# Kernel tuning notes

Hardware: AMD Instinct MI355X
Metric: run time of the kernel (lower is better)

## Reference

```python
import jax, jax.numpy as jnp
import numpy as np

B, T, D, S, EXP = 4, 2048, 1024, 16, 2
E = D * EXP  # expanded channels = 2048


def setup_inputs() -> dict:
    key = jax.random.key(0)
    ks = jax.random.split(key, 8)
    s = 0.02
    f = jnp.float32
    return {
        "x": jax.random.normal(ks[0], (B, T, D), f),
        "in_w": jax.random.normal(ks[1], (2 * E, D), f) * s,
        "in_b": jnp.zeros((2 * E,), f),
        "conv_w": jax.random.normal(ks[2], (E, 1, 3), f) * s,  # depthwise conv, groups=E
        "conv_b": jnp.zeros((E,), f),
        "dt_w": jax.random.normal(ks[3], (E, E), f) * s,
        "dt_b": jnp.zeros((E,), f),
        "B_w": jax.random.normal(ks[4], (S, E), f) * s,
        "B_b": jnp.zeros((S,), f),
        "C_w": jax.random.normal(ks[5], (S, E), f) * s,
        "C_b": jnp.zeros((S,), f),
        "D_w": jax.random.normal(ks[6], (S, E), f) * s,
        "D_b": jnp.zeros((S,), f),
        "out_w": jax.random.normal(ks[7], (D, E), f) * s,
        "out_b": jnp.zeros((D,), f),
    }


def reference(x, in_w, in_b, conv_w, conv_b, dt_w, dt_b, B_w, B_b, C_w, C_b, D_w, D_b, out_w, out_b):
    silu = jax.nn.silu
    # in_proj -> split into main / gate, each [B,T,E]
    xp = x @ in_w.T + in_b
    x_main, x_gate = xp[..., :E], xp[..., E:]
    # depthwise temporal conv (kernel 3, pad 1, groups=E), then SiLU
    xc = jax.lax.conv_general_dilated(
        x_main.transpose(0, 2, 1), conv_w, (1,), [(1, 1)],
        dimension_numbers=("NCH", "OIH", "NCH"), feature_group_count=E)
    xc = silu((xc + conv_b[None, :, None]).transpose(0, 2, 1))  # [B,T,E]
    dt = jax.nn.softplus(xc @ dt_w.T + dt_b)                     # [B,T,E]
    Bt = xc @ B_w.T + B_b                                        # [B,T,S]
    Ct = xc @ C_w.T + C_b
    Dt = xc @ D_w.T + D_b
    decay = jnp.exp(jnp.clip(-dt.mean(-1), -10.0, 10.0))         # [B,T] scalar decay per step
    u = Bt * Dt                                                  # [B,T,S] state input

    def step(state, inp):  # state [B,S]
        d, u_t, c_t = inp
        state = state * d[:, None] + u_t
        return state, (c_t * state).sum(-1)  # y_t [B]

    _, ys = jax.lax.scan(step, jnp.zeros((x.shape[0], S), x.dtype),
                         (decay.T, u.transpose(1, 0, 2), Ct.transpose(1, 0, 2)))
    y = ys.T[..., None] * silu(x_gate)  # broadcast [B,T,1] -> [B,T,E] (matches .expand)
    return x + (y @ out_w.T + out_b)    # dropout in eval mode = identity
```

## Files before the change

### kernel.cpp

```cpp
#include <hip/hip_runtime.h>
#include <hip/hip_bf16.h>

#define Bsz 4
#define Tsz 2048
#define Dsz 1024
#define Ssz 16
#define Esz 2048
#define Mrows (Bsz*Tsz)

typedef __attribute__((ext_vector_type(8))) short short8;
typedef __attribute__((ext_vector_type(4))) float floatx4;
typedef __attribute__((ext_vector_type(8))) int int8v;
typedef __attribute__((ext_vector_type(4))) int int4v;

__device__ __forceinline__ void async_ld16(const void* g, void* l) {
    __builtin_amdgcn_global_load_lds(
        (const __attribute__((address_space(1))) void*)g,
        (__attribute__((address_space(3))) void*)l,
        16, 0, 0);
}

__device__ __forceinline__ float sigmoidf_(float v) { return 1.f / (1.f + expf(-v)); }
__device__ __forceinline__ float bf2f(unsigned short u) {
    union { unsigned u32; float f; } c; c.u32 = (unsigned)u << 16; return c.f;
}
__device__ __forceinline__ int pk_fp8x4(float a, float b, float c, float d) {
    int lo = __builtin_amdgcn_cvt_pk_fp8_f32(a, b, 0, 0);
    int hi = __builtin_amdgcn_cvt_pk_fp8_f32(c, d, 0, 0);
    return (lo & 0xFFFF) | (hi << 16);
}

#define WAIT_VM(N)   (0xF70 | (N))
#define WAIT_LGKM(N) (0xC07F | ((N) << 8))

#define CV_S0 2097152
#define CV_S1 3145728
#define CV_S2 4194304
#define CV_S3 4718592
__global__ void cvt_all(const float4* __restrict__ x,  const float4* __restrict__ iw,
                        const float4* __restrict__ dw, const float4* __restrict__ ow,
                        int* __restrict__ x8, int* __restrict__ iw8,
                        int* __restrict__ dw8, int* __restrict__ ow8) {
    int i = blockIdx.x * blockDim.x + threadIdx.x;
    const int stride = gridDim.x * blockDim.x;
    for (; i < CV_S3; i += stride) {
        if (i < CV_S0) {
            float4 v = x[i];
            x8[i] = pk_fp8x4(v.x, v.y, v.z, v.w);
        } else if (i < CV_S1) {
            const int j = i - CV_S0;
            float4 v = iw[j];
            iw8[j] = pk_fp8x4(v.x * 64.f, v.y * 64.f, v.z * 64.f, v.w * 64.f);
        } else if (i < CV_S2) {
            const int j = i - CV_S1;
            float4 v = dw[j];
            dw8[j] = pk_fp8x4(v.x * 64.f, v.y * 64.f, v.z * 64.f, v.w * 64.f);
        } else {
            const int j = i - CV_S2;
            float4 v = ow[j];
            ow8[j] = pk_fp8x4(v.x * 64.f, v.y * 64.f, v.z * 64.f, v.w * 64.f);
        }
    }
}

template<int MODE, int SA, int SB>
__launch_bounds__(256, 2)
__global__ void gemm_f8(const unsigned char* __restrict__ A,
                        const unsigned char* __restrict__ Bw,
                        const float* __restrict__ bias,
                        int M, int N, int K,
                        __hip_bfloat16* __restrict__ outb,
                        float* __restrict__ rowsum,
                        const float* __restrict__ resid,
                        const float* __restrict__ ysv,
                        float* __restrict__ outf) {
    __shared__ __align__(16) unsigned char sA[2 * 16384];
    __shared__ __align__(16) unsigned char sB[2 * 16384];

    const int tid  = threadIdx.x;
    const int wave = tid >> 6, lane = tid & 63;
    const int wm = wave >> 1, wn = wave & 1;
    const int q = lane >> 4, lr = lane & 15;

    const int gx = gridDim.x, gy = gridDim.y;
    const int flat = blockIdx.y * gx + blockIdx.x;
    const int stripe = gy >> 3;
    const int xcd = flat & 7, local = flat >> 3;
    const int mt = xcd * stripe + (local % stripe);
    const int nt = local / stripe;
    const int m0 = mt * 128, n0 = nt * 128;

    floatx4 acc[4][4];
#pragma unroll
    for (int i = 0; i < 4; ++i)
#pragma unroll
        for (int j = 0; j < 4; ++j) acc[i][j] = (floatx4){0.f, 0.f, 0.f, 0.f};

    const unsigned char* pa[4];
    const unsigned char* pb[4];
#pragma unroll
    for (int i = 0; i < 4; ++i) {
        const int idx = i * 256 + tid, row = idx >> 3, s = idx & 7;
        pa[i] = A + (size_t)(m0 + row) * K + ((s ^ (row & 7)) * 16);
        pb[i] = Bw + (size_t)(n0 + row) * K + ((s ^ (row & 7)) * 16);
    }

    const int rA = wm * 64 + lr, rB = wn * 64 + lr;
    const int oA0 = rA * 128 + (((2 * q)     ^ (rA & 7)) * 16);
    const int oA1 = rA * 128 + (((2 * q + 1) ^ (rA & 7)) * 16);
    const int oB0 = rB * 128 + (((2 * q)     ^ (rB & 7)) * 16);
    const int oB1 = rB * 128 + (((2 * q + 1) ^ (rB & 7)) * 16);

#define F8_ISSUE(ST) do {                                                      \
        _Pragma("unroll")                                                      \
        for (int i = 0; i < 4; ++i) {                                          \
            async_ld16(pa[i], &sA[(ST) * 16384 + (i * 256 + wave * 64) * 16]); \
            pa[i] += 128;                                                      \
        }                                                                      \
        _Pragma("unroll")                                                      \
        for (int i = 0; i < 4; ++i) {                                          \
            async_ld16(pb[i], &sB[(ST) * 16384 + (i * 256 + wave * 64) * 16]); \
            pb[i] += 128;                                                      \
        }                                                                      \
    } while (0)

#define F8_STEP(ST) do {                                                       \
        asm volatile("" ::: "memory");                                         \
        __builtin_amdgcn_s_waitcnt(WAIT_VM(8));          \
        __builtin_amdgcn_s_barrier();                                          \
        asm volatile("" ::: "memory");                                         \
        int8v a8[4], b8[4];                                                    \
        _Pragma("unroll")                                                      \
        for (int i = 0; i < 4; ++i) {                                          \
            int4v lo = *(const int4v*)&sA[(ST) * 16384 + oA0 + i * 2048];      \
            int4v hi = *(const int4v*)&sA[(ST) * 16384 + oA1 + i * 2048];      \
            a8[i] = __builtin_shufflevector(lo, hi, 0, 1, 2, 3, 4, 5, 6, 7);   \
        }                                                                      \
        _Pragma("unroll")                                                      \
        for (int j = 0; j < 4; ++j) {                                          \
            int4v lo = *(const int4v*)&sB[(ST) * 16384 + oB0 + j * 2048];      \
            int4v hi = *(const int4v*)&sB[(ST) * 16384 + oB1 + j * 2048];      \
            b8[j] = __builtin_shufflevector(lo, hi, 0, 1, 2, 3, 4, 5, 6, 7);   \
        }                                                                      \
        asm volatile("" ::: "memory");                                         \
        __builtin_amdgcn_s_waitcnt(WAIT_LGKM(0));            \
        __builtin_amdgcn_s_barrier();                      \
        asm volatile("" ::: "memory");                                         \
        F8_ISSUE(ST);                               \
        _Pragma("unroll")                                                      \
        for (int i = 0; i < 4; ++i)                                            \
            _Pragma("unroll")                                                  \
            for (int j = 0; j < 4; ++j)                                        \
                acc[i][j] = __builtin_amdgcn_mfma_scale_f32_16x16x128_f8f6f4(  \
                    a8[i], b8[j], acc[i][j], 0, 0, 0, SA, 0, SB);              \
    } while (0)

    const int nit = K >> 8;
    F8_ISSUE(0);
    F8_ISSUE(1);
    for (int it = 0; it < nit; ++it) {
        F8_STEP(0);
        F8_STEP(1);
    }
#undef F8_STEP
#undef F8_ISSUE
    asm volatile("" ::: "memory");
    __builtin_amdgcn_s_waitcnt(WAIT_VM(0));

    if (MODE == 0) {
#pragma unroll
        for (int i = 0; i < 4; ++i) {
            const int row = m0 + wm * 64 + i * 16 + q * 4;
#pragma unroll
            for (int j = 0; j < 4; ++j) {
                const int col = n0 + wn * 64 + j * 16 + lr;
                const float bc = bias[col];
#pragma unroll
                for (int r = 0; r < 4; ++r)
                    outb[(size_t)(row + r) * N + col] = __float2bfloat16(acc[i][j][r] + bc);
            }
        }
    } else if (MODE == 1) {
#pragma unroll
        for (int i = 0; i < 4; ++i) {
            float rs[4] = {0.f, 0.f, 0.f, 0.f};
#pragma unroll
            for (int j = 0; j < 4; ++j) {
                const int col = n0 + wn * 64 + j * 16 + lr;
                const float bc = bias[col];
#pragma unroll
                for (int r = 0; r < 4; ++r) {
                    float v = acc[i][j][r] + bc;
                    float sp = (v > 20.f) ? v : log1pf(expf(v));
                    rs[r] += sp;
                }
            }
#pragma unroll
            for (int r = 0; r < 4; ++r) {
                float v = rs[r];
                v += __shfl_xor(v, 1); v += __shfl_xor(v, 2);
                v += __shfl_xor(v, 4); v += __shfl_xor(v, 8);
                if (lr == 0)
                    atomicAdd(&rowsum[m0 + wm * 64 + i * 16 + q * 4 + r], v);
            }
        }
    } else {
#pragma unroll
        for (int i = 0; i < 4; ++i) {
            const int row = m0 + wm * 64 + i * 16 + q * 4;
#pragma unroll
            for (int j = 0; j < 4; ++j) {
                const int col = n0 + wn * 64 + j * 16 + lr;
                const float bc = bias[col];
#pragma unroll
                for (int r = 0; r < 4; ++r) {
                    const size_t idx = (size_t)(row + r) * N + col;
                    outf[idx] = resid[idx] + ysv[row + r] * acc[i][j][r] + bc;
                }
            }
        }
    }
}

__global__ void conv_gate_k(const __hip_bfloat16* __restrict__ xp,
                            const float* __restrict__ cw,
                            const float* __restrict__ cb,
                            __hip_bfloat16* __restrict__ xc,
                            int2* __restrict__ xc8,
                            int2* __restrict__ s8) {
    const int idx8 = blockIdx.x * blockDim.x + threadIdx.x;
    const int e = (idx8 & (Esz / 8 - 1)) * 8;
    const int r = idx8 >> 8;
    const int t = r & (Tsz - 1);
    const unsigned short* row0 = (const unsigned short*)(xp + (size_t)r * (2 * Esz) + e);
    short8 vm1 = (t > 0)       ? *(const short8*)(row0 - 2 * Esz) : (short8){0,0,0,0,0,0,0,0};
    short8 v00 = *(const short8*)row0;
    short8 vp1 = (t < Tsz - 1) ? *(const short8*)(row0 + 2 * Esz) : (short8){0,0,0,0,0,0,0,0};
    short8 o;
    float sil[8];
#pragma unroll
    for (int k = 0; k < 8; ++k) {
        const int ek = e + k;
        float v = bf2f((unsigned short)vm1[k]) * cw[ek * 3 + 0]
                + bf2f((unsigned short)v00[k]) * cw[ek * 3 + 1]
                + bf2f((unsigned short)vp1[k]) * cw[ek * 3 + 2] + cb[ek];
        sil[k] = v * sigmoidf_(v);
        __hip_bfloat16 h = __float2bfloat16(sil[k]);
        o[k] = *(short*)&h;
    }
    *(short8*)(xc + (size_t)idx8 * 8) = o;
    int2 p;
    p.x = pk_fp8x4(sil[0] * 16.f, sil[1] * 16.f, sil[2] * 16.f, sil[3] * 16.f);
    p.y = pk_fp8x4(sil[4] * 16.f, sil[5] * 16.f, sil[6] * 16.f, sil[7] * 16.f);
    xc8[idx8] = p;

    short8 g = *(const short8*)(row0 + Esz);
    float sg[8];
#pragma unroll
    for (int k = 0; k < 8; ++k) {
        const float gv = bf2f((unsigned short)g[k]);
        sg[k] = gv * sigmoidf_(gv);
    }
    int2 ps;
    ps.x = pk_fp8x4(sg[0] * 16.f, sg[1] * 16.f, sg[2] * 16.f, sg[3] * 16.f);
    ps.y = pk_fp8x4(sg[4] * 16.f, sg[5] * 16.f, sg[6] * 16.f, sg[7] * 16.f);
    s8[idx8] = ps;
}

__global__ void pack_bcd(const float* __restrict__ Bw, const float* __restrict__ Cw,
                         const float* __restrict__ Dw, __hip_bfloat16* __restrict__ Wb) {
    const int idx = blockIdx.x * blockDim.x + threadIdx.x;
    if (idx >= 48 * Esz) return;
    const int row = idx >> 11, col = idx & (Esz - 1);
    float v;
    if (row < 16)      v = Bw[row * Esz + col];
    else if (row < 32) v = Cw[(row - 16) * Esz + col];
    else               v = Dw[(row - 32) * Esz + col];
    Wb[idx] = __float2bfloat16(v);
}

__launch_bounds__(128)
__global__ void bcd_mfma2(const __hip_bfloat16* __restrict__ xc,
                          const __hip_bfloat16* __restrict__ Wb,
                          const float* __restrict__ Bb, const float* __restrict__ Cb,
                          const float* __restrict__ Db,
                          float* __restrict__ u, float* __restrict__ Ct) {
    __shared__ __align__(16) __hip_bfloat16 sW[48 * 256];
    const int tid = threadIdx.x;
    const int wave = tid >> 6, lane = tid & 63;
    const int q = lane >> 4, lr = lane & 15;
    const int m0 = blockIdx.x * 32;

    floatx4 acc[3];
#pragma unroll
    for (int j = 0; j < 3; ++j) acc[j] = (floatx4){0.f, 0.f, 0.f, 0.f};

    const __hip_bfloat16* arow = xc + (size_t)(m0 + wave * 16 + lr) * Esz;

    for (int kt = 0; kt < 8; ++kt) {
        const int k0 = kt << 8;
        __syncthreads();
#pragma unroll
        for (int j = 0; j < 12; ++j) {
            const int idx = j * 128 + tid;
            const int row = idx >> 5, ch = idx & 31;
            async_ld16(&Wb[(size_t)row * Esz + k0 + ch * 8],
                       (__hip_bfloat16*)sW + idx * 8);
        }
        __builtin_amdgcn_s_waitcnt(WAIT_VM(0));
        __syncthreads();

        short8 af[8];
#pragma unroll
        for (int ks = 0; ks < 8; ++ks)
            af[ks] = *(const short8*)&arow[k0 + ks * 32 + q * 8];
#pragma unroll
        for (int ks = 0; ks < 8; ++ks) {
#pragma unroll
            for (int j = 0; j < 3; ++j) {
                short8 wf = *(const short8*)&sW[(j * 16 + lr) * 256 + ks * 32 + q * 8];
                acc[j] = __builtin_amdgcn_mfma_f32_16x16x32_bf16(af[ks], wf, acc[j], 0, 0, 0);
            }
        }
    }

    const int row = m0 + wave * 16 + q * 4;
    const float bb = Bb[lr], cbv = Cb[lr], db = Db[lr];
#pragma unroll
    for (int r = 0; r < 4; ++r) {
        const float bt = acc[0][r] + bb;
        const float ct = acc[1][r] + cbv;
        const float dt = acc[2][r] + db;
        u [(size_t)(row + r) * Ssz + lr] = bt * dt;
        Ct[(size_t)(row + r) * Ssz + lr] = ct;
    }
}

__global__ void scanA(const float* __restrict__ rowsum, const float* __restrict__ u,
                      const float* __restrict__ Ct,
                      float* __restrict__ ysl, float* __restrict__ pt,
                      float* __restrict__ send) {
    const int cid = blockIdx.x;
    const int b = cid >> 3, c = cid & 7;
    const int t0 = c * 256;
    const int tid = threadIdx.x;
    const int lane = tid & 63, wave = tid >> 6;
    __shared__ __align__(16) float su[256 * Ssz];
    __shared__ __align__(16) float sc[256 * Ssz];
    __shared__ float sp[256 * 17];
    __shared__ float sd[256];

    const float4* ub = (const float4*)(u  + ((size_t)b * Tsz + t0) * Ssz);
    const float4* cb = (const float4*)(Ct + ((size_t)b * Tsz + t0) * Ssz);
#pragma unroll
    for (int i = 0; i < 4; ++i) {
        ((float4*)su)[tid + i * 256] = ub[tid + i * 256];
        ((float4*)sc)[tid + i * 256] = cb[tid + i * 256];
    }
    {
        const float m = rowsum[b * Tsz + t0 + tid] * (1.f / (float)Esz);
        sd[tid] = expf(fminf(fmaxf(-m, -10.f), 10.f));
    }
    __syncthreads();
    if (wave == 0 && lane < 16) {
        float st = 0.f, P = 1.f;
#pragma unroll 8
        for (int i = 0; i < 256; ++i) {
            const float d = sd[i];
            st = st * d + su[i * Ssz + lane];
            sp[i * 17 + lane] = sc[i * Ssz + lane] * st;
            if (lane == 0) { P *= d; sp[i * 17 + 16] = P; }
        }
        send[cid * Ssz + lane] = st;
    }
    __syncthreads();
    float s = 0.f;
#pragma unroll
    for (int j = 0; j < 16; ++j) s += sp[tid * 17 + j];
    ysl[b * Tsz + t0 + tid] = s;
    pt [b * Tsz + t0 + tid] = sp[tid * 17 + 16];
}

__global__ void scanB(const float* __restrict__ send, const float* __restrict__ pt,
                      float* __restrict__ sstart) {
    const int tid = threadIdx.x;
    if (tid >= 64) return;
    const int b = tid >> 4, j = tid & 15;
    float s = 0.f;
    for (int c = 0; c < 8; ++c) {
        const int cid = b * 8 + c;
        sstart[cid * Ssz + j] = s;
        const float Pc = pt[b * Tsz + c * 256 + 255];
        s = send[cid * Ssz + j] + Pc * s;
    }
}

__global__ void scanC(const float* __restrict__ ysl, const float* __restrict__ pt,
                      const float* __restrict__ sstart, const float* __restrict__ Ct,
                      float* __restrict__ ys) {
    const int cid = blockIdx.x;
    const int b = cid >> 3, c = cid & 7;
    const int t0 = c * 256;
    const int tid = threadIdx.x;
    __shared__ float s0[Ssz];
    if (tid < 16) s0[tid] = sstart[cid * Ssz + tid];
    __syncthreads();
    const int g = b * Tsz + t0 + tid;
    const float4* cr = (const float4*)(Ct + (size_t)g * Ssz);
    float dot = 0.f;
#pragma unroll
    for (int i = 0; i < 4; ++i) {
        float4 v = cr[i];
        dot += v.x * s0[i * 4 + 0] + v.y * s0[i * 4 + 1]
             + v.z * s0[i * 4 + 2] + v.w * s0[i * 4 + 3];
    }
    ys[g] = ysl[g] + pt[g] * dot;
}

extern "C" void kernel_launch(void* const* d_in, const int* in_sizes, int n_in,
                              void* d_out, int out_size, void* d_ws, size_t ws_size,
                              hipStream_t stream) {
    const float* x      = (const float*)d_in[0];
    const float* in_w   = (const float*)d_in[1];
    const float* in_b   = (const float*)d_in[2];
    const float* conv_w = (const float*)d_in[3];
    const float* conv_b = (const float*)d_in[4];
    const float* dt_w   = (const float*)d_in[5];
    const float* dt_b   = (const float*)d_in[6];
    const float* B_w    = (const float*)d_in[7];
    const float* B_b    = (const float*)d_in[8];
    const float* C_w    = (const float*)d_in[9];
    const float* C_b    = (const float*)d_in[10];
    const float* D_w    = (const float*)d_in[11];
    const float* D_b    = (const float*)d_in[12];
    const float* out_w  = (const float*)d_in[13];
    const float* out_b  = (const float*)d_in[14];
    float* out = (float*)d_out;

    char* ws = (char*)d_ws;
    auto alloc = [&](size_t bytes) {
        char* p = ws;
        ws += (bytes + 255) & ~(size_t)255;
        return p;
    };
    unsigned char* x_f8    = (unsigned char*)alloc((size_t)Mrows * Dsz);
    unsigned char* inw_f8  = (unsigned char*)alloc((size_t)2 * Esz * Dsz);
    unsigned char* dtw_f8  = (unsigned char*)alloc((size_t)Esz * Esz);
    unsigned char* outw_f8 = (unsigned char*)alloc((size_t)Dsz * Esz);
    __hip_bfloat16* xp_bf  = (__hip_bfloat16*)alloc((size_t)Mrows * 2 * Esz * 2);
    __hip_bfloat16* xc_bf  = (__hip_bfloat16*)alloc((size_t)Mrows * Esz * 2);
    unsigned char* xc_f8   = (unsigned char*)alloc((size_t)Mrows * Esz);
    unsigned char* s_f8    = (unsigned char*)alloc((size_t)Mrows * Esz);
    __hip_bfloat16* wb_bf  = (__hip_bfloat16*)alloc((size_t)48 * Esz * 2);
    float* rowsum = (float*)alloc(Mrows * 4);
    float* u_buf  = (float*)alloc((size_t)Mrows * Ssz * 4);
    float* ct_buf = (float*)alloc((size_t)Mrows * Ssz * 4);
    float* ys_buf = (float*)alloc(Mrows * 4);
    float* ysl_buf = (float*)alloc(Mrows * 4);
    float* pt_buf  = (float*)alloc(Mrows * 4);
    float* send_buf = (float*)alloc(32 * Ssz * 4);
    float* sstart_buf = (float*)alloc(32 * Ssz * 4);
    (void)alloc(65536);

    hipMemsetAsync(rowsum, 0, Mrows * 4, stream);

    cvt_all<<<4608, 256, 0, stream>>>((const float4*)x, (const float4*)in_w,
                                      (const float4*)dt_w, (const float4*)out_w,
                                      (int*)x_f8, (int*)inw_f8, (int*)dtw_f8,
                                      (int*)outw_f8);
    pack_bcd<<<48 * Esz / 256, 256, 0, stream>>>(B_w, C_w, D_w, wb_bf);

    gemm_f8<0, 127, 121><<<dim3(4096 / 128, Mrows / 128), 256, 0, stream>>>(
        x_f8, inw_f8, in_b, Mrows, 4096, 1024, xp_bf, nullptr, nullptr, nullptr, nullptr);

    conv_gate_k<<<(Mrows * Esz / 8) / 256, 256, 0, stream>>>(
        xp_bf, conv_w, conv_b, xc_bf, (int2*)xc_f8, (int2*)s_f8);

    gemm_f8<1, 123, 121><<<dim3(Esz / 128, Mrows / 128), 256, 0, stream>>>(
        xc_f8, dtw_f8, dt_b, Mrows, Esz, Esz, nullptr, rowsum, nullptr, nullptr, nullptr);

    bcd_mfma2<<<Mrows / 32, 128, 0, stream>>>(xc_bf, wb_bf, B_b, C_b, D_b, u_buf, ct_buf);

    scanA<<<32, 256, 0, stream>>>(rowsum, u_buf, ct_buf, ysl_buf, pt_buf, send_buf);
    scanB<<<1, 64, 0, stream>>>(send_buf, pt_buf, sstart_buf);
    scanC<<<32, 256, 0, stream>>>(ysl_buf, pt_buf, sstart_buf, ct_buf, ys_buf);

    gemm_f8<2, 123, 121><<<dim3(Dsz / 128, Mrows / 128), 256, 0, stream>>>(
        s_f8, outw_f8, out_b, Mrows, Dsz, Esz, nullptr, nullptr, x, ys_buf, out);
}
```

Before: 385.7 us.

## Fuse gate SiLU into in_proj epilogue, merge weight packing and scan passes

The in_proj GEMM now writes only the main half as bf16 and applies SiLU plus fp8 quantisation to the gate half directly in its epilogue. This removes the bf16 round trip of the gate columns and the gate work in the conv kernel. The B/C/D weight packing is folded into the conversion kernel, and the single-block scanB is removed by having each scanC block recompute its chunk start state serially. The changes cut kernel launches and intermediate memory traffic. The cost is byte-wide scattered fp8 stores in the GEMM epilogue.

New measurement: 380.6 us. Within noise of the previous version (-1.3%).

```diff
diff --git a/kernel.cpp b/kernel.cpp
--- a/kernel.cpp
+++ b/kernel.cpp
@@ -12,6 +12,7 @@
 typedef __attribute__((ext_vector_type(4))) float floatx4;
 typedef __attribute__((ext_vector_type(8))) int int8v;
 typedef __attribute__((ext_vector_type(4))) int int4v;
+typedef __attribute__((ext_vector_type(4))) unsigned short ushort4v;
 
 __device__ __forceinline__ void async_ld16(const void* g, void* l) {
     __builtin_amdgcn_global_load_lds(
@@ -24,6 +25,10 @@
 __device__ __forceinline__ float bf2f(unsigned short u) {
     union { unsigned u32; float f; } c; c.u32 = (unsigned)u << 16; return c.f;
 }
+__device__ __forceinline__ unsigned short f2bf(float f) {
+    __hip_bfloat16 h = __float2bfloat16(f);
+    return *(unsigned short*)&h;
+}
 __device__ __forceinline__ int pk_fp8x4(float a, float b, float c, float d) {
     int lo = __builtin_amdgcn_cvt_pk_fp8_f32(a, b, 0, 0);
     int hi = __builtin_amdgcn_cvt_pk_fp8_f32(c, d, 0, 0);
@@ -37,13 +42,17 @@
 #define CV_S1 3145728
 #define CV_S2 4194304
 #define CV_S3 4718592
+#define CV_S4 4743168
 __global__ void cvt_all(const float4* __restrict__ x,  const float4* __restrict__ iw,
                         const float4* __restrict__ dw, const float4* __restrict__ ow,
+                        const float4* __restrict__ Bw, const float4* __restrict__ Cw,
+                        const float4* __restrict__ Dw,
                         int* __restrict__ x8, int* __restrict__ iw8,
-                        int* __restrict__ dw8, int* __restrict__ ow8) {
+                        int* __restrict__ dw8, int* __restrict__ ow8,
+                        ushort4v* __restrict__ wb) {
     int i = blockIdx.x * blockDim.x + threadIdx.x;
     const int stride = gridDim.x * blockDim.x;
-    for (; i < CV_S3; i += stride) {
+    for (; i < CV_S4; i += stride) {
         if (i < CV_S0) {
             float4 v = x[i];
             x8[i] = pk_fp8x4(v.x, v.y, v.z, v.w);
@@ -55,10 +64,19 @@
             const int j = i - CV_S1;
             float4 v = dw[j];
             dw8[j] = pk_fp8x4(v.x * 64.f, v.y * 64.f, v.z * 64.f, v.w * 64.f);
-        } else {
+        } else if (i < CV_S3) {
             const int j = i - CV_S2;
             float4 v = ow[j];
             ow8[j] = pk_fp8x4(v.x * 64.f, v.y * 64.f, v.z * 64.f, v.w * 64.f);
+        } else {
+            const int j = i - CV_S3;
+            float4 v;
+            if (j < 8192)       v = Bw[j];
+            else if (j < 16384) v = Cw[j - 8192];
+            else                v = Dw[j - 16384];
+            ushort4v o;
+            o[0] = f2bf(v.x); o[1] = f2bf(v.y); o[2] = f2bf(v.z); o[3] = f2bf(v.w);
+            wb[j] = o;
         }
     }
 }
@@ -73,7 +91,8 @@
                         float* __restrict__ rowsum,
                         const float* __restrict__ resid,
                         const float* __restrict__ ysv,
-                        float* __restrict__ outf) {
+                        float* __restrict__ outf,
+                        unsigned char* __restrict__ gate8) {
     __shared__ __align__(16) unsigned char sA[2 * 16384];
     __shared__ __align__(16) unsigned char sB[2 * 16384];
 
@@ -204,7 +223,7 @@
                     atomicAdd(&rowsum[m0 + wm * 64 + i * 16 + q * 4 + r], v);
             }
         }
-    } else {
+    } else if (MODE == 2) {
 #pragma unroll
         for (int i = 0; i < 4; ++i) {
             const int row = m0 + wm * 64 + i * 16 + q * 4;
@@ -219,23 +238,56 @@
                 }
             }
         }
-    }
-}
-
-__global__ void conv_gate_k(const __hip_bfloat16* __restrict__ xp,
+    } else {
+        if (nt < 16) {
+#pragma unroll
+            for (int i = 0; i < 4; ++i) {
+                const int row = m0 + wm * 64 + i * 16 + q * 4;
+#pragma unroll
+                for (int j = 0; j < 4; ++j) {
+                    const int col = n0 + wn * 64 + j * 16 + lr;
+                    const float bc = bias[col];
+#pragma unroll
+                    for (int r = 0; r < 4; ++r)
+                        outb[(size_t)(row + r) * Esz + col] =
+                            __float2bfloat16(acc[i][j][r] + bc);
+                }
+            }
+        } else {
+#pragma unroll
+            for (int i = 0; i < 4; ++i) {
+                const int row = m0 + wm * 64 + i * 16 + q * 4;
+#pragma unroll
+                for (int j = 0; j < 4; ++j) {
+                    const int col = n0 + wn * 64 + j * 16 + lr;
+                    const float bc = bias[col];
+                    const int colg = col - Esz;
+#pragma unroll
+                    for (int r = 0; r < 4; ++r) {
+                        const float v = acc[i][j][r] + bc;
+                        const float sil = v * sigmoidf_(v) * 16.f;
+                        const int pk = __builtin_amdgcn_cvt_pk_fp8_f32(sil, sil, 0, 0);
+                        gate8[(size_t)(row + r) * Esz + colg] = (unsigned char)(pk & 0xFF);
+                    }
+                }
+            }
+        }
+    }
+}
+
+__global__ void conv_gate_k(const __hip_bfloat16* __restrict__ xpm,
                             const float* __restrict__ cw,
                             const float* __restrict__ cb,
                             __hip_bfloat16* __restrict__ xc,
-                            int2* __restrict__ xc8,
-                            int2* __restrict__ s8) {
+                            int2* __restrict__ xc8) {
     const int idx8 = blockIdx.x * blockDim.x + threadIdx.x;
     const int e = (idx8 & (Esz / 8 - 1)) * 8;
     const int r = idx8 >> 8;
     const int t = r & (Tsz - 1);
-    const unsigned short* row0 = (const unsigned short*)(xp + (size_t)r * (2 * Esz) + e);
-    short8 vm1 = (t > 0)       ? *(const short8*)(row0 - 2 * Esz) : (short8){0,0,0,0,0,0,0,0};
+    const unsigned short* row0 = (const unsigned short*)(xpm + (size_t)r * Esz + e);
+    short8 vm1 = (t > 0)       ? *(const short8*)(row0 - Esz) : (short8){0,0,0,0,0,0,0,0};
     short8 v00 = *(const short8*)row0;
-    short8 vp1 = (t < Tsz - 1) ? *(const short8*)(row0 + 2 * Esz) : (short8){0,0,0,0,0,0,0,0};
+    short8 vp1 = (t < Tsz - 1) ? *(const short8*)(row0 + Esz) : (short8){0,0,0,0,0,0,0,0};
     short8 o;
     float sil[8];
 #pragma unroll
@@ -245,38 +297,13 @@
                 + bf2f((unsigned short)v00[k]) * cw[ek * 3 + 1]
                 + bf2f((unsigned short)vp1[k]) * cw[ek * 3 + 2] + cb[ek];
         sil[k] = v * sigmoidf_(v);
-        __hip_bfloat16 h = __float2bfloat16(sil[k]);
-        o[k] = *(short*)&h;
+        o[k] = (short)f2bf(sil[k]);
     }
     *(short8*)(xc + (size_t)idx8 * 8) = o;
     int2 p;
     p.x = pk_fp8x4(sil[0] * 16.f, sil[1] * 16.f, sil[2] * 16.f, sil[3] * 16.f);
     p.y = pk_fp8x4(sil[4] * 16.f, sil[5] * 16.f, sil[6] * 16.f, sil[7] * 16.f);
     xc8[idx8] = p;
-
-    short8 g = *(const short8*)(row0 + Esz);
-    float sg[8];
-#pragma unroll
-    for (int k = 0; k < 8; ++k) {
-        const float gv = bf2f((unsigned short)g[k]);
-        sg[k] = gv * sigmoidf_(gv);
-    }
-    int2 ps;
-    ps.x = pk_fp8x4(sg[0] * 16.f, sg[1] * 16.f, sg[2] * 16.f, sg[3] * 16.f);
-    ps.y = pk_fp8x4(sg[4] * 16.f, sg[5] * 16.f, sg[6] * 16.f, sg[7] * 16.f);
-    s8[idx8] = ps;
-}
-
-__global__ void pack_bcd(const float* __restrict__ Bw, const float* __restrict__ Cw,
-                         const float* __restrict__ Dw, __hip_bfloat16* __restrict__ Wb) {
-    const int idx = blockIdx.x * blockDim.x + threadIdx.x;
-    if (idx >= 48 * Esz) return;
-    const int row = idx >> 11, col = idx & (Esz - 1);
-    float v;
-    if (row < 16)      v = Bw[row * Esz + col];
-    else if (row < 32) v = Cw[(row - 16) * Esz + col];
-    else               v = Dw[(row - 32) * Esz + col];
-    Wb[idx] = __float2bfloat16(v);
 }
 
 __launch_bounds__(128)
@@ -381,29 +408,22 @@
     pt [b * Tsz + t0 + tid] = sp[tid * 17 + 16];
 }
 
-__global__ void scanB(const float* __restrict__ send, const float* __restrict__ pt,
-                      float* __restrict__ sstart) {
-    const int tid = threadIdx.x;
-    if (tid >= 64) return;
-    const int b = tid >> 4, j = tid & 15;
-    float s = 0.f;
-    for (int c = 0; c < 8; ++c) {
-        const int cid = b * 8 + c;
-        sstart[cid * Ssz + j] = s;
-        const float Pc = pt[b * Tsz + c * 256 + 255];
-        s = send[cid * Ssz + j] + Pc * s;
-    }
-}
-
 __global__ void scanC(const float* __restrict__ ysl, const float* __restrict__ pt,
-                      const float* __restrict__ sstart, const float* __restrict__ Ct,
+                      const float* __restrict__ send, const float* __restrict__ Ct,
                       float* __restrict__ ys) {
     const int cid = blockIdx.x;
     const int b = cid >> 3, c = cid & 7;
     const int t0 = c * 256;
     const int tid = threadIdx.x;
     __shared__ float s0[Ssz];
-    if (tid < 16) s0[tid] = sstart[cid * Ssz + tid];
+    if (tid < 16) {
+        float s = 0.f;
+        for (int cc = 0; cc < c; ++cc) {
+            const float Pc = pt[(b * 8 + cc) * 256 + 255];
+            s = send[(b * 8 + cc) * Ssz + tid] + Pc * s;
+        }
+        s0[tid] = s;
+    }
     __syncthreads();
     const int g = b * Tsz + t0 + tid;
     const float4* cr = (const float4*)(Ct + (size_t)g * Ssz);
@@ -447,7 +467,7 @@
     unsigned char* inw_f8  = (unsigned char*)alloc((size_t)2 * Esz * Dsz);
     unsigned char* dtw_f8  = (unsigned char*)alloc((size_t)Esz * Esz);
     unsigned char* outw_f8 = (unsigned char*)alloc((size_t)Dsz * Esz);
-    __hip_bfloat16* xp_bf  = (__hip_bfloat16*)alloc((size_t)Mrows * 2 * Esz * 2);
+    __hip_bfloat16* xpm_bf = (__hip_bfloat16*)alloc((size_t)Mrows * Esz * 2);
     __hip_bfloat16* xc_bf  = (__hip_bfloat16*)alloc((size_t)Mrows * Esz * 2);
     unsigned char* xc_f8   = (unsigned char*)alloc((size_t)Mrows * Esz);
     unsigned char* s_f8    = (unsigned char*)alloc((size_t)Mrows * Esz);
@@ -459,32 +479,34 @@
     float* ysl_buf = (float*)alloc(Mrows * 4);
     float* pt_buf  = (float*)alloc(Mrows * 4);
     float* send_buf = (float*)alloc(32 * Ssz * 4);
-    float* sstart_buf = (float*)alloc(32 * Ssz * 4);
     (void)alloc(65536);
 
     hipMemsetAsync(rowsum, 0, Mrows * 4, stream);
 
     cvt_all<<<4608, 256, 0, stream>>>((const float4*)x, (const float4*)in_w,
                                       (const float4*)dt_w, (const float4*)out_w,
+                                      (const float4*)B_w, (const float4*)C_w,
+                                      (const float4*)D_w,
                                       (int*)x_f8, (int*)inw_f8, (int*)dtw_f8,
-                                      (int*)outw_f8);
-    pack_bcd<<<48 * Esz / 256, 256, 0, stream>>>(B_w, C_w, D_w, wb_bf);
-
-    gemm_f8<0, 127, 121><<<dim3(4096 / 128, Mrows / 128), 256, 0, stream>>>(
-        x_f8, inw_f8, in_b, Mrows, 4096, 1024, xp_bf, nullptr, nullptr, nullptr, nullptr);
+                                      (int*)outw_f8, (ushort4v*)wb_bf);
+
+    gemm_f8<3, 127, 121><<<dim3(4096 / 128, Mrows / 128), 256, 0, stream>>>(
+        x_f8, inw_f8, in_b, Mrows, 4096, 1024, xpm_bf, nullptr, nullptr, nullptr,
+        nullptr, s_f8);
 
     conv_gate_k<<<(Mrows * Esz / 8) / 256, 256, 0, stream>>>(
-        xp_bf, conv_w, conv_b, xc_bf, (int2*)xc_f8, (int2*)s_f8);
+        xpm_bf, conv_w, conv_b, xc_bf, (int2*)xc_f8);
 
     gemm_f8<1, 123, 121><<<dim3(Esz / 128, Mrows / 128), 256, 0, stream>>>(
-        xc_f8, dtw_f8, dt_b, Mrows, Esz, Esz, nullptr, rowsum, nullptr, nullptr, nullptr);
+        xc_f8, dtw_f8, dt_b, Mrows, Esz, Esz, nullptr, rowsum, nullptr, nullptr,
+        nullptr, nullptr);
 
     bcd_mfma2<<<Mrows / 32, 128, 0, stream>>>(xc_bf, wb_bf, B_b, C_b, D_b, u_buf, ct_buf);
 
     scanA<<<32, 256, 0, stream>>>(rowsum, u_buf, ct_buf, ysl_buf, pt_buf, send_buf);
-    scanB<<<1, 64, 0, stream>>>(send_buf, pt_buf, sstart_buf);
-    scanC<<<32, 256, 0, stream>>>(ysl_buf, pt_buf, sstart_buf, ct_buf, ys_buf);
+    scanC<<<32, 256, 0, stream>>>(ysl_buf, pt_buf, send_buf, ct_buf, ys_buf);
 
     gemm_f8<2, 123, 121><<<dim3(Dsz / 128, Mrows / 128), 256, 0, stream>>>(
-        s_f8, outw_f8, out_b, Mrows, Dsz, Esz, nullptr, nullptr, x, ys_buf, out);
-}
+        s_f8, outw_f8, out_b, Mrows, Dsz, Esz, nullptr, nullptr, x, ys_buf, out,
+        nullptr);
+}
```
